# Kernel optimization log

Hardware: AMD Instinct MI355X
Metric: run time of the kernel (lower is better)

The kernel has to match this reference:

```python
import jax, jax.numpy as jnp
import numpy as np

EMBED_DIM = 1024
NUM_HEADS = 16
HEAD_DIM = EMBED_DIM // NUM_HEADS


def setup_inputs() -> dict:
    key = jax.random.key(0)
    k1, k2, k3, k4, k5 = jax.random.split(key, 5)
    B, N, C = 4, 2048, EMBED_DIM
    s = 1.0 / np.sqrt(C)
    return {
        "x": jax.random.normal(k1, (B, N, C), dtype=jnp.float32),
        "w_qkv": jax.random.uniform(k2, (C, 3 * C), dtype=jnp.float32, minval=-s, maxval=s),
        "b_qkv": jax.random.uniform(k3, (3 * C,), dtype=jnp.float32, minval=-s, maxval=s),
        "w_out": jax.random.uniform(k4, (C, C), dtype=jnp.float32, minval=-s, maxval=s),
        "b_out": jax.random.uniform(k5, (C,), dtype=jnp.float32, minval=-s, maxval=s),
    }


def reference(x, w_qkv, b_qkv, w_out, b_out):
    B, N, C = x.shape
    H, D = NUM_HEADS, HEAD_DIM
    qkv = x @ w_qkv + b_qkv                       # [B, N, 3C]
    qkv = qkv.reshape(B, N, 3, H, D)
    q = qkv[:, :, 0].transpose(0, 2, 1, 3)        # [B, H, N, D]
    k = qkv[:, :, 1].transpose(0, 2, 1, 3)
    v = qkv[:, :, 2].transpose(0, 2, 1, 3)
    scale = 1.0 / np.sqrt(D).astype(np.float32)
    attn = jnp.einsum('bhnd,bhmd->bhnm', q, k) * scale  # [B, H, N, N]
    attn = jax.nn.softmax(attn, axis=-1)
    out = jnp.einsum('bhnm,bhmd->bhnd', attn, v)  # [B, H, N, D]
    out = out.transpose(0, 2, 1, 3).reshape(B, N, C)
    return out @ w_out + b_out
```

## Files before the change

kernel.cpp:

```cpp
#include <hip/hip_runtime.h>


typedef unsigned short u16;
typedef unsigned long long u64;
typedef __bf16 bf16x8 __attribute__((ext_vector_type(8)));
typedef float f32x4 __attribute__((ext_vector_type(4)));
typedef unsigned int u32x2 __attribute__((ext_vector_type(2)));

#define MFMA(a, b, c) __builtin_amdgcn_mfma_f32_16x16x32_bf16(a, b, c, 0, 0, 0)

#define QSCALE 0.18033688011112043f

__device__ __forceinline__ u16 f2bf(float f) {
    __bf16 h = (__bf16)f;
    return *(u16*)&h;
}

__device__ __forceinline__ float fexp2(float x) {
#if __has_builtin(__builtin_amdgcn_exp2f)
    return __builtin_amdgcn_exp2f(x);
#else
    return __expf(x * 0.6931471805599453f);
#endif
}

__device__ __forceinline__ void gld16(const void* g, void* l) {
    __builtin_amdgcn_global_load_lds(
        (const __attribute__((address_space(1))) void*)g,
        (__attribute__((address_space(3))) void*)l, 16, 0, 0);
}

__device__ __forceinline__ void bar()      { __asm__ volatile("s_barrier" ::: "memory"); }
__device__ __forceinline__ void wait_vm6() { __asm__ volatile("s_waitcnt vmcnt(6)" ::: "memory"); }
__device__ __forceinline__ void wait_vm0() { __asm__ volatile("s_waitcnt vmcnt(0)" ::: "memory"); }

__global__ __launch_bounds__(256) void cvt_f32_bf16(
    const float* __restrict__ src, u16* __restrict__ dst, long n)
{
    long i = ((long)blockIdx.x * 256 + threadIdx.x) * 8;
    if (i >= n) return;
    float4 a = *(const float4*)&src[i];
    float4 b = *(const float4*)&src[i + 4];
    union { u16 u[8]; uint4 v; } tmp;
    tmp.u[0] = f2bf(a.x); tmp.u[1] = f2bf(a.y);
    tmp.u[2] = f2bf(a.z); tmp.u[3] = f2bf(a.w);
    tmp.u[4] = f2bf(b.x); tmp.u[5] = f2bf(b.y);
    tmp.u[6] = f2bf(b.z); tmp.u[7] = f2bf(b.w);
    *(uint4*)&dst[i] = tmp.v;
}

__global__ __launch_bounds__(256) void transpose_f2b(
    const float* __restrict__ src, u16* __restrict__ dst, int R, int C)
{
    __shared__ alignas(16) u16 tile[64 * 80];
    const int r0 = blockIdx.y * 64, c0 = blockIdx.x * 64;
    const int t = threadIdx.x;
#pragma unroll
    for (int c = 0; c < 4; c++) {
        int idx = t + c * 256;
        int r = idx >> 4, seg = idx & 15;
        float4 f = *(const float4*)&src[(long)(r0 + r) * C + c0 + seg * 4];
        u16* p = &tile[r * 80 + seg * 4];
        p[0] = f2bf(f.x); p[1] = f2bf(f.y); p[2] = f2bf(f.z); p[3] = f2bf(f.w);
    }
    __syncthreads();
#pragma unroll
    for (int c = 0; c < 2; c++) {
        int idx = t + c * 256;
        int rr = idx >> 3, seg = idx & 7;
        union { u16 u[8]; uint4 v; } tmp;
#pragma unroll
        for (int j = 0; j < 8; j++) tmp.u[j] = tile[(seg * 8 + j) * 80 + rr];
        *(uint4*)&dst[(long)(c0 + rr) * R + r0 + seg * 8] = tmp.v;
    }
}

template <int EPI>
__global__ __launch_bounds__(512, 1) void gemm_bf16(
    const u16* __restrict__ A, const u16* __restrict__ Bt,
    const float* __restrict__ bias,
    u16* __restrict__ out0, u16* __restrict__ out1, u16* __restrict__ out2,
    float* __restrict__ outf,
    int M, int N, int K)
{
    const int m0 = blockIdx.x * 256, n0 = blockIdx.y * 128;
    const int t = threadIdx.x;
    const int wave = t >> 6, lane = t & 63, quad = lane >> 4, l15 = lane & 15;
    const int wm = wave >> 1, wn = wave & 1;

    __shared__ alignas(16) u16 As[3][16384];
    __shared__ alignas(16) u16 Bs[3][8192];

    const int sr = lane >> 3;
    const int sc8 = ((lane & 7) ^ sr) * 8;

    const int rx = l15 & 7;
    int arow[4], brow[4];
#pragma unroll
    for (int ft = 0; ft < 4; ft++) {
        arow[ft] = (wm * 64 + ft * 16 + l15) * 64;
        brow[ft] = (wn * 64 + ft * 16 + l15) * 64;
    }
    const int xoff[2] = { ((0 * 4 + quad) ^ rx) * 8, ((1 * 4 + quad) ^ rx) * 8 };

    const int NT = K >> 6;

#define STAGE_A(kt_, slot_, o_)                                               \
    gld16(&A[(long)(m0 + (o_) * 64 + wave * 8 + sr) * K + ((kt_) << 6) + sc8],\
          &As[slot_][(o_) * 4096 + wave * 512])
#define STAGE_B(kt_, slot_, o_)                                               \
    gld16(&Bt[(long)(n0 + (o_) * 64 + wave * 8 + sr) * K + ((kt_) << 6) + sc8],\
          &Bs[slot_][(o_) * 4096 + wave * 512])

#pragma unroll
    for (int s = 0; s < 2; s++) {
        STAGE_A(s, s, 0); STAGE_A(s, s, 1); STAGE_A(s, s, 2); STAGE_A(s, s, 3);
        STAGE_B(s, s, 0); STAGE_B(s, s, 1);
    }
    wait_vm6();
    bar();

    f32x4 acc[4][4] = {};
    int cur = 0, c2 = 2;

    for (int kt = 0; kt < NT; kt++) {
        const u16* Ac = As[cur];
        const u16* Bc = Bs[cur];
        const bool st = (kt + 2 < NT);

#pragma unroll
        for (int ks = 0; ks < 2; ks++) {
            bf16x8 af[4], bf[4];
#pragma unroll
            for (int ft = 0; ft < 4; ft++) {
                af[ft] = *(const bf16x8*)&Ac[arow[ft] + xoff[ks]];
                bf[ft] = *(const bf16x8*)&Bc[brow[ft] + xoff[ks]];
            }
            if (st) {
                if (ks == 0) { STAGE_A(kt + 2, c2, 0); STAGE_A(kt + 2, c2, 1);
                               STAGE_A(kt + 2, c2, 2); }
                else         { STAGE_A(kt + 2, c2, 3);
                               STAGE_B(kt + 2, c2, 0); STAGE_B(kt + 2, c2, 1); }
            }
            bar();
            __builtin_amdgcn_s_setprio(1);
#pragma unroll
            for (int mt = 0; mt < 4; mt++)
#pragma unroll
                for (int nt = 0; nt < 4; nt++)
                    acc[mt][nt] = MFMA(bf[nt], af[mt], acc[mt][nt]);
            __builtin_amdgcn_s_setprio(0);
            if (ks == 1) {
                if (st)               wait_vm6();
                else if (kt + 1 < NT) wait_vm0();
            }
            bar();
        }
        cur = (cur == 2) ? 0 : cur + 1;
        c2  = (c2 == 2) ? 0 : c2 + 1;
    }
#undef STAGE_A
#undef STAGE_B

#pragma unroll
    for (int mt = 0; mt < 4; mt++) {
        int token = m0 + wm * 64 + mt * 16 + l15;
        int bb = token >> 11, nn = token & 2047;
#pragma unroll
        for (int nt = 0; nt < 4; nt++) {
            int cgb = n0 + wn * 64 + nt * 16 + quad * 4;
            float4 bv = *(const float4*)&bias[cgb];
            float v0 = acc[mt][nt][0] + bv.x;
            float v1 = acc[mt][nt][1] + bv.y;
            float v2 = acc[mt][nt][2] + bv.z;
            float v3 = acc[mt][nt][3] + bv.w;
            if (EPI == 0) {
                int t3 = cgb >> 10;
                int hh = (cgb >> 6) & 15, dd = cgb & 63;
                int bh = (bb << 4) + hh;
                if (t3 == 0) {
                    union { u16 u[4]; u64 v; } pk;
                    pk.u[0] = f2bf(v0 * QSCALE); pk.u[1] = f2bf(v1 * QSCALE);
                    pk.u[2] = f2bf(v2 * QSCALE); pk.u[3] = f2bf(v3 * QSCALE);
                    *(u64*)&out0[((long)bh * 2048 + nn) * 64 + dd] = pk.v;
                } else if (t3 == 1) {
                    union { u16 u[4]; u64 v; } pk;
                    pk.u[0] = f2bf(v0); pk.u[1] = f2bf(v1);
                    pk.u[2] = f2bf(v2); pk.u[3] = f2bf(v3);
                    *(u64*)&out1[((long)bh * 2048 + nn) * 64 + dd] = pk.v;
                } else {
                    long vbo = ((long)bh * 64 + dd) * 2048 + nn;
                    out2[vbo]            = f2bf(v0);
                    out2[vbo + 2048]     = f2bf(v1);
                    out2[vbo + 2 * 2048] = f2bf(v2);
                    out2[vbo + 3 * 2048] = f2bf(v3);
                }
            } else {
                float4 o4 = { v0, v1, v2, v3 };
                *(float4*)&outf[(long)token * N + cgb] = o4;
            }
        }
    }
}

__global__ __launch_bounds__(256, 2) void flash_attn(
    const u16* __restrict__ q, const u16* __restrict__ k,
    const u16* __restrict__ vt, u16* __restrict__ attn)
{
    const int bh = blockIdx.x;
    const int b = bh >> 4, h = bh & 15;
    const int q0 = blockIdx.y * 256;
    const int t = threadIdx.x;
    const int wave = t >> 6, lane = t & 63, quad = lane >> 4, l15 = lane & 15;

    __shared__ alignas(16) u16 Ks[2][4096];
    __shared__ alignas(16) u16 Vs[2][4096];

    const u16* kb = k + (long)bh * 2048 * 64;
    const u16* vb = vt + (long)bh * 64 * 2048;

    bf16x8 qf[4][2];
#pragma unroll
    for (int mt = 0; mt < 4; mt++) {
        long row = (long)bh * 2048 + q0 + wave * 64 + mt * 16 + l15;
        qf[mt][0] = *(const bf16x8*)&q[row * 64 + quad * 8];
        qf[mt][1] = *(const bf16x8*)&q[row * 64 + 32 + quad * 8];
    }

    bf16x8 ones;
#pragma unroll
    for (int j = 0; j < 8; j++) ones[j] = (__bf16)1.0f;

    const int ri = lane >> 3;
    const int ci = (lane & 7) ^ ri;
    const int sg = wave * 2;

    const int lperm = (l15 & 3) | ((l15 & 4) << 1) | ((l15 & 8) >> 1);
    const int swk = (quad ^ (lperm & 7)) * 8;
    const int swv = (quad ^ (l15 & 7)) * 8;

    const int koff0 = lperm * 64 + swk;
    const int koff1 = lperm * 64 + (swk ^ 32);
    const int voff[2] = { l15 * 64 + swv, l15 * 64 + (swv ^ 32) };

    f32x4 o[4][4] = {};
    f32x4 ls[4] = {};

    const u16* kp0 = kb + (long)((sg + 0) * 8 + ri) * 64 + ci * 8;
    const u16* kp1 = kb + (long)((sg + 1) * 8 + ri) * 64 + ci * 8;
    const u16* vp0 = vb + (long)((sg + 0) * 8 + ri) * 2048 + ci * 8;
    const u16* vp1 = vb + (long)((sg + 1) * 8 + ri) * 2048 + ci * 8;

    gld16(kp0, &Ks[0][(sg + 0) * 512]);
    gld16(kp1, &Ks[0][(sg + 1) * 512]);
    gld16(vp0, &Vs[0][(sg + 0) * 512]);
    gld16(vp1, &Vs[0][(sg + 1) * 512]);
    kp0 += 4096; kp1 += 4096; vp0 += 64; vp1 += 64;

    for (int kt2 = 0; kt2 < 16; kt2++) {
#pragma unroll
        for (int half = 0; half < 2; half++) {
            const int cur = half;
            const bool stage_next = (half == 0) | (kt2 < 15);

            __syncthreads();

            if (stage_next) {
                gld16(kp0, &Ks[cur ^ 1][(sg + 0) * 512]);
                gld16(kp1, &Ks[cur ^ 1][(sg + 1) * 512]);
                gld16(vp0, &Vs[cur ^ 1][(sg + 0) * 512]);
                gld16(vp1, &Vs[cur ^ 1][(sg + 1) * 512]);
                kp0 += 4096; kp1 += 4096; vp0 += 64; vp1 += 64;
            }

            f32x4 st[4][4];
            __builtin_amdgcn_s_setprio(1);
#pragma unroll
            for (int ct = 0; ct < 4; ct++) {
                bf16x8 kf0 = *(const bf16x8*)&Ks[cur][ct * 1024 + koff0];
                bf16x8 kf1 = *(const bf16x8*)&Ks[cur][ct * 1024 + koff1];
#pragma unroll
                for (int mt = 0; mt < 4; mt++) {
                    f32x4 z = {};
                    z = MFMA(kf0, qf[mt][0], z);
                    st[mt][ct] = MFMA(kf1, qf[mt][1], z);
                }
            }
            __builtin_amdgcn_s_setprio(0);

#pragma unroll
            for (int hp = 0; hp < 2; hp++) {
                bf16x8 va[4];
#pragma unroll
                for (int dt = 0; dt < 4; dt++)
                    va[dt] = *(const bf16x8*)&Vs[cur][dt * 1024 + voff[hp]];

                bf16x8 pb[4];
#pragma unroll
                for (int mt = 0; mt < 4; mt++) {
                    unsigned w[2][2];
#pragma unroll
                    for (int c = 0; c < 2; c++)
#pragma unroll
                        for (int p = 0; p < 2; p++) {
                            u16 lo = f2bf(fexp2(st[mt][2 * hp + c][2 * p]));
                            u16 hi = f2bf(fexp2(st[mt][2 * hp + c][2 * p + 1]));
                            w[c][p] = (unsigned)lo | ((unsigned)hi << 16);
                        }
                    u32x2 pa0 = __builtin_amdgcn_permlane32_swap(
                        w[0][0], w[1][0], false, false);
                    u32x2 pa1 = __builtin_amdgcn_permlane32_swap(
                        w[0][1], w[1][1], false, false);
                    union { unsigned d[4]; bf16x8 v; } uu;
                    uu.d[0] = pa0[0];
                    uu.d[1] = pa1[0];
                    uu.d[2] = pa0[1];
                    uu.d[3] = pa1[1];
                    pb[mt] = uu.v;
                }

                __builtin_amdgcn_s_setprio(1);
#pragma unroll
                for (int mt = 0; mt < 4; mt++)
                    ls[mt] = MFMA(ones, pb[mt], ls[mt]);
#pragma unroll
                for (int dt = 0; dt < 4; dt++)
#pragma unroll
                    for (int mt = 0; mt < 4; mt++)
                        o[mt][dt] = MFMA(va[dt], pb[mt], o[mt][dt]);
                __builtin_amdgcn_s_setprio(0);
            }
        }
    }

#pragma unroll
    for (int mt = 0; mt < 4; mt++) {
        float inv = 1.f / ls[mt][0];
        int n = q0 + wave * 64 + mt * 16 + l15;
#pragma unroll
        for (int dt = 0; dt < 4; dt++) {
            union { u16 u[4]; u64 v; } pk;
#pragma unroll
            for (int r = 0; r < 4; r++) pk.u[r] = f2bf(o[mt][dt][r] * inv);
            *(u64*)&attn[((long)b * 2048 + n) * 1024 + h * 64 + dt * 16 + quad * 4] =
                pk.v;
        }
    }
}

extern "C" void kernel_launch(void* const* d_in, const int* in_sizes, int n_in,
                              void* d_out, int out_size, void* d_ws, size_t ws_size,
                              hipStream_t stream) {
    const float* x     = (const float*)d_in[0];
    const float* w_qkv = (const float*)d_in[1];
    const float* b_qkv = (const float*)d_in[2];
    const float* w_out = (const float*)d_in[3];
    const float* b_out = (const float*)d_in[4];
    float* out = (float*)d_out;

    u16* ws    = (u16*)d_ws;
    u16* q     = ws;
    u16* kk    = q + 8388608;
    u16* vt    = kk + 8388608;
    u16* attn  = vt + 8388608;
    u16* x_bf  = attn + 8388608;
    u16* wqkvT = x_bf + 8388608;
    u16* woutT = wqkvT + 3145728;

    cvt_f32_bf16<<<4096, 256, 0, stream>>>(x, x_bf, 8388608L);
    transpose_f2b<<<dim3(48, 16), 256, 0, stream>>>(w_qkv, wqkvT, 1024, 3072);
    transpose_f2b<<<dim3(16, 16), 256, 0, stream>>>(w_out, woutT, 1024, 1024);
    gemm_bf16<0><<<dim3(32, 24), 512, 0, stream>>>(x_bf, wqkvT, b_qkv, q, kk, vt,
                                                   nullptr, 8192, 3072, 1024);
    flash_attn<<<dim3(64, 8), 256, 0, stream>>>(q, kk, vt, attn);
    gemm_bf16<1><<<dim3(32, 8), 512, 0, stream>>>(attn, woutT, b_out, nullptr,
                                                  nullptr, nullptr, out,
                                                  8192, 1024, 1024);
}
```

Before: 269.1 us.

## Split GEMM k-step into four MFMA phases with finer-grained staging

Restructures the bf16 GEMM main loop from two k-substeps into four phases, each loading a subset of B fragments and issuing a subset of the global-to-LDS stage loads before an 8-MFMA cluster. Explicit lgkmcnt(0) waits with sched_barrier replace compiler-chosen waits, and the LDS arrays are flattened to 1D with slot-based addressing. The aim is to interleave LDS reads, async global loads and MFMA work more evenly across waves. In exchange it doubles the number of barriers per k-tile, which may add synchronisation stalls.

```diff
diff --git a/kernel.cpp b/kernel.cpp
--- a/kernel.cpp
+++ b/kernel.cpp
@@ -33,6 +33,8 @@
 __device__ __forceinline__ void bar()      { __asm__ volatile("s_barrier" ::: "memory"); }
 __device__ __forceinline__ void wait_vm6() { __asm__ volatile("s_waitcnt vmcnt(6)" ::: "memory"); }
 __device__ __forceinline__ void wait_vm0() { __asm__ volatile("s_waitcnt vmcnt(0)" ::: "memory"); }
+__device__ __forceinline__ void lgkm0()    { __asm__ volatile("s_waitcnt lgkmcnt(0)" ::: "memory");
+                                             __builtin_amdgcn_sched_barrier(0); }
 
 __global__ __launch_bounds__(256) void cvt_f32_bf16(
     const float* __restrict__ src, u16* __restrict__ dst, long n)
@@ -88,8 +90,8 @@
     const int wave = t >> 6, lane = t & 63, quad = lane >> 4, l15 = lane & 15;
     const int wm = wave >> 1, wn = wave & 1;
 
-    __shared__ alignas(16) u16 As[3][16384];
-    __shared__ alignas(16) u16 Bs[3][8192];
+    __shared__ alignas(16) u16 As[3 * 16384];
+    __shared__ alignas(16) u16 Bs[3 * 8192];
 
     const int sr = lane >> 3;
     const int sc8 = ((lane & 7) ^ sr) * 8;
@@ -107,10 +109,10 @@
 
 #define STAGE_A(kt_, slot_, o_)                                               \
     gld16(&A[(long)(m0 + (o_) * 64 + wave * 8 + sr) * K + ((kt_) << 6) + sc8],\
-          &As[slot_][(o_) * 4096 + wave * 512])
+          &As[(slot_) * 16384 + ((o_) * 64 + wave * 8) * 64])
 #define STAGE_B(kt_, slot_, o_)                                               \
     gld16(&Bt[(long)(n0 + (o_) * 64 + wave * 8 + sr) * K + ((kt_) << 6) + sc8],\
-          &Bs[slot_][(o_) * 4096 + wave * 512])
+          &Bs[(slot_) * 8192 + ((o_) * 64 + wave * 8) * 64])
 
 #pragma unroll
     for (int s = 0; s < 2; s++) {
@@ -124,38 +126,69 @@
     int cur = 0, c2 = 2;
 
     for (int kt = 0; kt < NT; kt++) {
-        const u16* Ac = As[cur];
-        const u16* Bc = Bs[cur];
+        const u16* Ac = &As[cur * 16384];
+        const u16* Bc = &Bs[cur * 8192];
         const bool st = (kt + 2 < NT);
-
-#pragma unroll
-        for (int ks = 0; ks < 2; ks++) {
-            bf16x8 af[4], bf[4];
-#pragma unroll
-            for (int ft = 0; ft < 4; ft++) {
-                af[ft] = *(const bf16x8*)&Ac[arow[ft] + xoff[ks]];
-                bf[ft] = *(const bf16x8*)&Bc[brow[ft] + xoff[ks]];
-            }
-            if (st) {
-                if (ks == 0) { STAGE_A(kt + 2, c2, 0); STAGE_A(kt + 2, c2, 1);
-                               STAGE_A(kt + 2, c2, 2); }
-                else         { STAGE_A(kt + 2, c2, 3);
-                               STAGE_B(kt + 2, c2, 0); STAGE_B(kt + 2, c2, 1); }
-            }
-            bar();
-            __builtin_amdgcn_s_setprio(1);
-#pragma unroll
-            for (int mt = 0; mt < 4; mt++)
-#pragma unroll
-                for (int nt = 0; nt < 4; nt++)
-                    acc[mt][nt] = MFMA(bf[nt], af[mt], acc[mt][nt]);
-            __builtin_amdgcn_s_setprio(0);
-            if (ks == 1) {
-                if (st)               wait_vm6();
-                else if (kt + 1 < NT) wait_vm0();
-            }
-            bar();
-        }
+        bf16x8 af[4], bf[4];
+
+#pragma unroll
+        for (int ft = 0; ft < 4; ft++) af[ft] = *(const bf16x8*)&Ac[arow[ft] + xoff[0]];
+        bf[0] = *(const bf16x8*)&Bc[brow[0] + xoff[0]];
+        bf[1] = *(const bf16x8*)&Bc[brow[1] + xoff[0]];
+        if (st) { STAGE_A(kt + 2, c2, 0); STAGE_A(kt + 2, c2, 1); }
+        bar(); lgkm0();
+        __builtin_amdgcn_s_setprio(1);
+#pragma unroll
+        for (int mt = 0; mt < 4; mt++) {
+            acc[mt][0] = MFMA(bf[0], af[mt], acc[mt][0]);
+            acc[mt][1] = MFMA(bf[1], af[mt], acc[mt][1]);
+        }
+        __builtin_amdgcn_s_setprio(0);
+        bar();
+
+        bf[2] = *(const bf16x8*)&Bc[brow[2] + xoff[0]];
+        bf[3] = *(const bf16x8*)&Bc[brow[3] + xoff[0]];
+        if (st) STAGE_A(kt + 2, c2, 2);
+        bar(); lgkm0();
+        __builtin_amdgcn_s_setprio(1);
+#pragma unroll
+        for (int mt = 0; mt < 4; mt++) {
+            acc[mt][2] = MFMA(bf[2], af[mt], acc[mt][2]);
+            acc[mt][3] = MFMA(bf[3], af[mt], acc[mt][3]);
+        }
+        __builtin_amdgcn_s_setprio(0);
+        bar();
+
+#pragma unroll
+        for (int ft = 0; ft < 4; ft++) af[ft] = *(const bf16x8*)&Ac[arow[ft] + xoff[1]];
+        bf[0] = *(const bf16x8*)&Bc[brow[0] + xoff[1]];
+        bf[1] = *(const bf16x8*)&Bc[brow[1] + xoff[1]];
+        if (st) { STAGE_A(kt + 2, c2, 3); STAGE_B(kt + 2, c2, 0); }
+        bar(); lgkm0();
+        __builtin_amdgcn_s_setprio(1);
+#pragma unroll
+        for (int mt = 0; mt < 4; mt++) {
+            acc[mt][0] = MFMA(bf[0], af[mt], acc[mt][0]);
+            acc[mt][1] = MFMA(bf[1], af[mt], acc[mt][1]);
+        }
+        __builtin_amdgcn_s_setprio(0);
+        bar();
+
+        bf[2] = *(const bf16x8*)&Bc[brow[2] + xoff[1]];
+        bf[3] = *(const bf16x8*)&Bc[brow[3] + xoff[1]];
+        if (st) STAGE_B(kt + 2, c2, 1);
+        bar(); lgkm0();
+        __builtin_amdgcn_s_setprio(1);
+#pragma unroll
+        for (int mt = 0; mt < 4; mt++) {
+            acc[mt][2] = MFMA(bf[2], af[mt], acc[mt][2]);
+            acc[mt][3] = MFMA(bf[3], af[mt], acc[mt][3]);
+        }
+        __builtin_amdgcn_s_setprio(0);
+        if (st)                wait_vm6();
+        else if (kt + 2 == NT) wait_vm0();
+        bar();
+
         cur = (cur == 2) ? 0 : cur + 1;
         c2  = (c2 == 2) ? 0 : c2 + 1;
     }
```

Result: slower. 282.1 us (+4.8%).
